# Performance work log

Measured on AMD Instinct MI355X. Metric: run time of the kernel, lower is better.

Reference implementation:

```python
import jax, jax.numpy as jnp
import numpy as np

NUM_EXPERTS = 8
TOP_K = 2
HIDDEN = 1024
INTER = 3584
B, S = 1, 2048


def setup_inputs() -> dict:
    key = jax.random.key(0)
    k0, k1, k2, k3, k4 = jax.random.split(key, 5)
    scale = 0.02
    return {
        "hidden_states": jax.random.normal(k0, (B, S, HIDDEN), dtype=jnp.float32),
        "gate_w": jax.random.normal(k1, (NUM_EXPERTS, HIDDEN), dtype=jnp.float32) * scale,
        "w1": jax.random.normal(k2, (NUM_EXPERTS, INTER, HIDDEN), dtype=jnp.float32) * scale,
        "w2": jax.random.normal(k3, (NUM_EXPERTS, HIDDEN, INTER), dtype=jnp.float32) * scale,
        "w3": jax.random.normal(k4, (NUM_EXPERTS, INTER, HIDDEN), dtype=jnp.float32) * scale,
    }


def reference(hidden_states, gate_w, w1, w2, w3):
    b, s, h = hidden_states.shape
    x = hidden_states.reshape(-1, h)  # [T, H]
    T = x.shape[0]

    # Router: softmax in float32, take top-k, renormalize (normalize_routing_weights=1)
    router_logits = x @ gate_w.T  # [T, E]
    routing_probs = jax.nn.softmax(router_logits.astype(jnp.float32), axis=-1)
    top_w, top_i = jax.lax.top_k(routing_probs, TOP_K)  # [T, K]
    top_w = top_w / jnp.sum(top_w, axis=-1, keepdims=True)
    top_w = top_w.astype(x.dtype)

    # Dense per-token gate matrix [T, E]: weight if expert selected, else 0.
    rows = jnp.arange(T)[:, None]
    gates = jnp.zeros((T, NUM_EXPERTS), dtype=x.dtype).at[rows, top_i].set(top_w)

    # Equivalent to gather-MLP-scatter: y = sum_e gate[:,e] * SwiGLU_e(x)
    out = jnp.zeros((T, h), dtype=x.dtype)
    for e in range(NUM_EXPERTS):
        hid = jax.nn.silu(x @ w1[e].T) * (x @ w3[e].T)  # [T, F]
        out = out + (hid @ w2[e].T) * gates[:, e:e + 1]
    return out.reshape(b, s, h)
```

## Files before the change

### kernel.cpp

```cpp
#include <hip/hip_runtime.h>
#include <hip/hip_bf16.h>
#include <stdint.h>

#define T_TOKENS 2048
#define HID_DIM 1024
#define INTER 3584
#define NEXP 8
#define PTILES 40

typedef float f32x4 __attribute__((ext_vector_type(4)));
typedef short short8 __attribute__((ext_vector_type(8)));
typedef unsigned short ushort8 __attribute__((ext_vector_type(8)));

#define AS1 __attribute__((address_space(1)))
#define AS3 __attribute__((address_space(3)))

__device__ __forceinline__ void gload_lds16(const void* g, void* l) {
    __builtin_amdgcn_global_load_lds((AS1 void*)g, (AS3 void*)l, 16, 0, 0);
}

__device__ __forceinline__ f32x4 mfma16(short8 a, short8 b, f32x4 c) {
    return __builtin_amdgcn_mfma_f32_16x16x32_bf16(a, b, c, 0, 0, 0);
}

__device__ __forceinline__ unsigned short f2bf(float f) {
    union { __hip_bfloat16 h; unsigned short u; } cv;
    cv.h = __float2bfloat16(f);
    return cv.u;
}

__device__ __forceinline__ ushort8 cvt8(float4 v0, float4 v1) {
    ushort8 u;
    u[0] = f2bf(v0.x); u[1] = f2bf(v0.y); u[2] = f2bf(v0.z); u[3] = f2bf(v0.w);
    u[4] = f2bf(v1.x); u[5] = f2bf(v1.y); u[6] = f2bf(v1.z); u[7] = f2bf(v1.w);
    return u;
}

__global__ __launch_bounds__(256) void cvt_k(const float* __restrict__ w1, const float* __restrict__ w2,
                                             const float* __restrict__ w3,
                                             unsigned short* __restrict__ w1b,
                                             unsigned short* __restrict__ w2b,
                                             unsigned short* __restrict__ w3b) {
    const float* src;
    unsigned short* dst;
    if (blockIdx.z == 0) { src = w1; dst = w1b; }
    else if (blockIdx.z == 1) { src = w3; dst = w3b; }
    else { src = w2; dst = w2b; }
    size_t i = ((size_t)blockIdx.x * 256 + threadIdx.x) * 16;
    float4 v0 = *reinterpret_cast<const float4*>(src + i);
    float4 v1 = *reinterpret_cast<const float4*>(src + i + 4);
    float4 v2 = *reinterpret_cast<const float4*>(src + i + 8);
    float4 v3 = *reinterpret_cast<const float4*>(src + i + 12);
    *reinterpret_cast<ushort8*>(dst + i) = cvt8(v0, v1);
    *reinterpret_cast<ushort8*>(dst + i + 8) = cvt8(v2, v3);
}

__global__ void router_k(const float* __restrict__ x, const float* __restrict__ gw,
                         int* __restrict__ topk_e, float* __restrict__ topk_w,
                         int* __restrict__ ctl) {
    int lane = threadIdx.x & 63;
    int wid = threadIdx.x >> 6;
    int t = blockIdx.x * 4 + wid;
    const float* xr = x + (size_t)t * HID_DIM;

    float acc[NEXP];
#pragma unroll
    for (int e = 0; e < NEXP; ++e) acc[e] = 0.f;

#pragma unroll
    for (int j = 0; j < 4; ++j) {
        int c = j * 256 + lane * 4;
        float4 v = *reinterpret_cast<const float4*>(xr + c);
#pragma unroll
        for (int e = 0; e < NEXP; ++e) {
            float4 g = *reinterpret_cast<const float4*>(gw + e * HID_DIM + c);
            acc[e] += v.x * g.x + v.y * g.y + v.z * g.z + v.w * g.w;
        }
    }
#pragma unroll
    for (int off = 32; off > 0; off >>= 1)
#pragma unroll
        for (int e = 0; e < NEXP; ++e) acc[e] += __shfl_xor(acc[e], off, 64);

    if (lane == 0) {
        int e0 = 0;
#pragma unroll
        for (int e = 1; e < NEXP; ++e) if (acc[e] > acc[e0]) e0 = e;
        int e1 = -1;
        float b1 = 0.f;
#pragma unroll
        for (int e = 0; e < NEXP; ++e) {
            if (e == e0) continue;
            if (e1 < 0 || acc[e] > b1) { e1 = e; b1 = acc[e]; }
        }
        float p1 = __expf(b1 - acc[e0]);
        float s = 1.f + p1;
        topk_e[2 * t] = e0; topk_e[2 * t + 1] = e1;
        topk_w[2 * t] = 1.f / s; topk_w[2 * t + 1] = p1 / s;
        atomicAdd(&ctl[e0], 1);
        atomicAdd(&ctl[e1], 1);
    }
}

__global__ void prefix_k(int* __restrict__ ctl) {
    if (threadIdx.x == 0) {
        int r = 0, ns = 0;
        for (int e = 0; e < NEXP; ++e) {
            ctl[32 + e] = r;
            int c = ctl[e];
            r += (c + 127) & ~127;
            ctl[16 + e] = 0;
            int ntm = (c + 127) >> 7;
            for (int tm = 0; tm < ntm; ++tm) ctl[64 + ns++] = (e << 16) | tm;
        }
        ctl[48] = ns;
    }
}

__global__ void scatter_k(const int* __restrict__ topk_e, const float* __restrict__ topk_w,
                          int* __restrict__ ctl, int* __restrict__ perm_token,
                          float* __restrict__ perm_gate) {
    int t = blockIdx.x * 256 + threadIdx.x;
    if (t >= T_TOKENS) return;
#pragma unroll
    for (int k = 0; k < 2; ++k) {
        int e = topk_e[2 * t + k];
        int p = ctl[32 + e] + atomicAdd(&ctl[16 + e], 1);
        perm_token[p] = t;
        perm_gate[p] = topk_w[2 * t + k];
    }
}

__global__ __launch_bounds__(256) void pack_x_k(const float* __restrict__ x,
                                                const int* __restrict__ perm_token,
                                                unsigned short* __restrict__ xgp) {
    int ptile = blockIdx.x;
    int kt = blockIdx.y;
    int row = threadIdx.x & 127;
    int kh = threadIdx.x >> 7;
    int tok = perm_token[ptile * 128 + row];
    const float* s = x + (size_t)tok * HID_DIM + kt * 64 + kh * 32;
    unsigned short* d = xgp + (size_t)ptile * 131072 + (size_t)kt * 8192;
#pragma unroll
    for (int kb2 = 0; kb2 < 4; ++kb2) {
        int kb = kh * 4 + kb2;
        float4 v0 = *reinterpret_cast<const float4*>(s + kb2 * 8);
        float4 v1 = *reinterpret_cast<const float4*>(s + kb2 * 8 + 4);
        *reinterpret_cast<ushort8*>(d + (kb * 128 + row) * 8) = cvt8(v0, v1);
    }
}

__global__ __launch_bounds__(512, 4) void gemm1_k(
    const unsigned short* __restrict__ xgp,
    const unsigned short* __restrict__ w1b, const unsigned short* __restrict__ w3b,
    const int* __restrict__ ctl, unsigned short* __restrict__ hidp) {
    int ns = ctl[48];
    int nt = blockIdx.x >> 3;
    int slot = (blockIdx.x & 7) * 5 + blockIdx.y;
    if (slot >= ns) return;
    int et = ctl[64 + slot];
    int e = et >> 16, tm = et & 0xffff;
    int cnt = ctl[e];
    int off = ctl[32 + e];
    int ptile = (off >> 7) + tm;

    __shared__ __attribute__((aligned(16))) unsigned short A_l[8192];
    __shared__ __attribute__((aligned(16))) unsigned short B1_l[8192];
    __shared__ __attribute__((aligned(16))) unsigned short B3_l[8192];

    int tid = threadIdx.x;
    int lane = tid & 63;
    int wid = tid >> 6;
    int wr = wid >> 2, wc = wid & 3;
    int q = lane >> 4, rr = lane & 15;

    const unsigned short* asrc = xgp + (size_t)ptile * 131072;

    int col0 = tid >> 3;
    int c0 = tid & 7;
    int swzc = c0 ^ (col0 & 7);
    size_t rowbase = (size_t)(e * INTER + nt * 128) * HID_DIM;
    const unsigned short* b1r = w1b + rowbase + (size_t)col0 * HID_DIM + swzc * 8;
    const unsigned short* b3r = w3b + rowbase + (size_t)col0 * HID_DIM + swzc * 8;

    f32x4 acc1[4][2], acc3[4][2];
#pragma unroll
    for (int i = 0; i < 4; ++i)
#pragma unroll
        for (int j = 0; j < 2; ++j) { acc1[i][j] = 0.f; acc3[i][j] = 0.f; }

    for (int kt = 0; kt < 16; ++kt) {
        const unsigned short* as_ = asrc + (size_t)kt * 8192;
        gload_lds16(as_ + tid * 8, A_l + tid * 8);
        gload_lds16(as_ + (512 + tid) * 8, A_l + (512 + tid) * 8);
        gload_lds16(b1r + kt * 64, B1_l + tid * 8);
        gload_lds16(b1r + (size_t)64 * HID_DIM + kt * 64, B1_l + (512 + tid) * 8);
        gload_lds16(b3r + kt * 64, B3_l + tid * 8);
        gload_lds16(b3r + (size_t)64 * HID_DIM + kt * 64, B3_l + (512 + tid) * 8);
        __syncthreads();
#pragma unroll
        for (int kk = 0; kk < 2; ++kk) {
            short8 a[4], b1v[2], b3v[2];
            const unsigned short* abase = A_l + ((kk * 4 + q) * 128 + wr * 64 + rr) * 8;
#pragma unroll
            for (int i = 0; i < 4; ++i) a[i] = *reinterpret_cast<const short8*>(abase + i * 128);
            int swz = ((kk * 4 + q) ^ (rr & 7)) * 8;
            const unsigned short* b1base = B1_l + (wc * 32 + rr) * 64 + swz;
            const unsigned short* b3base = B3_l + (wc * 32 + rr) * 64 + swz;
#pragma unroll
            for (int j = 0; j < 2; ++j) {
                b1v[j] = *reinterpret_cast<const short8*>(b1base + j * 1024);
                b3v[j] = *reinterpret_cast<const short8*>(b3base + j * 1024);
            }
#pragma unroll
            for (int i = 0; i < 4; ++i)
#pragma unroll
                for (int j = 0; j < 2; ++j) {
                    acc1[i][j] = mfma16(a[i], b1v[j], acc1[i][j]);
                    acc3[i][j] = mfma16(a[i], b3v[j], acc3[i][j]);
                }
        }
        __syncthreads();
    }

    int rbase = wr * 64 + q * 4;
#pragma unroll
    for (int i = 0; i < 4; ++i) {
#pragma unroll
        for (int r = 0; r < 4; ++r) {
            int lrow = rbase + i * 16 + r;
            if (tm * 128 + lrow < cnt) {
#pragma unroll
                for (int j = 0; j < 2; ++j) {
                    int cw = wc * 32 + j * 16 + rr;
                    int tile = nt * 2 + (cw >> 6);
                    int cl = cw & 63;
                    float g = acc1[i][j][r];
                    float u = acc3[i][j][r];
                    float h = (g / (1.f + __expf(-g))) * u;
                    hidp[(size_t)(ptile * 56 + tile) * 8192 + ((cl >> 3) * 128 + lrow) * 8 + (cl & 7)] = f2bf(h);
                }
            }
        }
    }
}

__global__ __launch_bounds__(256) void gemm2_k(
    const unsigned short* __restrict__ hidp, const unsigned short* __restrict__ w2b,
    const int* __restrict__ ctl, const int* __restrict__ perm_token,
    const float* __restrict__ perm_gate, float* __restrict__ out) {
    int ns = ctl[48];
    int nty = blockIdx.x >> 3;
    int slot = (blockIdx.x & 7) * 5 + blockIdx.y;
    if (slot >= ns) return;
    int et = ctl[64 + slot];
    int e = et >> 16, tm = et & 0xffff;
    int ks = blockIdx.z;
    int cnt = ctl[e];
    int off = ctl[32 + e];
    int ptile = (off >> 7) + tm;

    __shared__ __attribute__((aligned(16))) unsigned short A_l[8192];
    __shared__ __attribute__((aligned(16))) unsigned short B_l[8192];

    int tid = threadIdx.x;
    int lane = tid & 63;
    int wid = tid >> 6;
    int wr = wid >> 1, wc = wid & 1;
    int q = lane >> 4, rr = lane & 15;

    const unsigned short* asrc = hidp + (size_t)(ptile * 56) * 8192;

    int colg0 = tid >> 3;
    int c0 = tid & 7;
    int swzc = c0 ^ (colg0 & 7);
    const unsigned short* b2r = w2b + (size_t)(e * HID_DIM + nty * 128 + colg0) * INTER + swzc * 8;

    f32x4 acc[4][4];
#pragma unroll
    for (int i = 0; i < 4; ++i)
#pragma unroll
        for (int j = 0; j < 4; ++j) acc[i][j] = 0.f;

    int kt0 = ks * 28;
    for (int t = 0; t < 28; ++t) {
        int kt = kt0 + t;
        const unsigned short* as_ = asrc + (size_t)kt * 8192;
#pragma unroll
        for (int c = 0; c < 4; ++c)
            gload_lds16(as_ + (c * 256 + tid) * 8, A_l + (c * 256 + tid) * 8);
#pragma unroll
        for (int i = 0; i < 4; ++i)
            gload_lds16(b2r + (size_t)i * 32 * INTER + kt * 64, B_l + (i * 256 + tid) * 8);
        __syncthreads();
#pragma unroll
        for (int kk = 0; kk < 2; ++kk) {
            short8 a[4], b[4];
            const unsigned short* abase = A_l + ((kk * 4 + q) * 128 + wr * 64 + rr) * 8;
            int swz = ((kk * 4 + q) ^ (rr & 7)) * 8;
            const unsigned short* bbase = B_l + wc * 4096 + rr * 64 + swz;
#pragma unroll
            for (int i = 0; i < 4; ++i) a[i] = *reinterpret_cast<const short8*>(abase + i * 128);
#pragma unroll
            for (int j = 0; j < 4; ++j) b[j] = *reinterpret_cast<const short8*>(bbase + j * 1024);
#pragma unroll
            for (int i = 0; i < 4; ++i)
#pragma unroll
                for (int j = 0; j < 4; ++j) acc[i][j] = mfma16(a[i], b[j], acc[i][j]);
        }
        __syncthreads();
    }

    int rb = wr * 64 + q * 4;
    int hb = nty * 128 + wc * 64 + rr;
#pragma unroll
    for (int i = 0; i < 4; ++i) {
#pragma unroll
        for (int r = 0; r < 4; ++r) {
            int lrow = rb + i * 16 + r;
            int grow = tm * 128 + lrow;
            if (grow < cnt) {
                int p = off + grow;
                int tok = perm_token[p];
                float gate = perm_gate[p];
#pragma unroll
                for (int j = 0; j < 4; ++j)
                    atomicAdd(&out[(size_t)tok * HID_DIM + hb + j * 16], acc[i][j][r] * gate);
            }
        }
    }
}

extern "C" void kernel_launch(void* const* d_in, const int* in_sizes, int n_in,
                              void* d_out, int out_size, void* d_ws, size_t ws_size,
                              hipStream_t stream) {
    const float* x  = (const float*)d_in[0];
    const float* gw = (const float*)d_in[1];
    const float* w1 = (const float*)d_in[2];
    const float* w2 = (const float*)d_in[3];
    const float* w3 = (const float*)d_in[4];
    float* out = (float*)d_out;

    char* ws = (char*)d_ws;
    int*   ctl        = (int*)ws;
    int*   topk_e     = (int*)(ws + 4096);
    float* topk_w     = (float*)(ws + 20480);
    int*   perm_token = (int*)(ws + 36864);
    float* perm_gate  = (float*)(ws + 57344);
    unsigned short* xgp  = (unsigned short*)(ws + (1ull << 20));
    unsigned short* hidp = (unsigned short*)(ws + 12582912);
    unsigned short* w1b  = (unsigned short*)(ws + 52428800);
    unsigned short* w3b  = (unsigned short*)(ws + 111149056);
    unsigned short* w2b  = (unsigned short*)(ws + 169869312);

    hipMemsetAsync(ctl, 0, 512, stream);
    hipMemsetAsync(perm_token, 0, PTILES * 128 * sizeof(int), stream);
    hipMemsetAsync(out, 0, (size_t)out_size * sizeof(float), stream);

    cvt_k<<<dim3(7168, 1, 3), 256, 0, stream>>>(w1, w2, w3, w1b, w2b, w3b);
    router_k<<<dim3(T_TOKENS / 4), 256, 0, stream>>>(x, gw, topk_e, topk_w, ctl);
    prefix_k<<<dim3(1), 64, 0, stream>>>(ctl);
    scatter_k<<<dim3(T_TOKENS / 256), 256, 0, stream>>>(topk_e, topk_w, ctl, perm_token, perm_gate);
    pack_x_k<<<dim3(PTILES, 16), 256, 0, stream>>>(x, perm_token, xgp);
    gemm1_k<<<dim3(224, 5), 512, 0, stream>>>(xgp, w1b, w3b, ctl, hidp);
    gemm2_k<<<dim3(64, 5, 2), 256, 0, stream>>>(hidp, w2b, ctl, perm_token, perm_gate, out);
}
```

Before: 341.0 us.

## Double-buffer LDS in both expert GEMMs with half-depth K steps and more split-K

Both expert GEMM kernels now use two LDS buffers, each holding a 32-wide K slice. Each step issues the global-to-LDS load for the next slice before computing on the current one, and a manual vmcnt wait plus raw s_barrier replaces the full __syncthreads pair. The B tile layout drops the XOR swizzle for a plain 32-element row stride, and launch bounds are raised for occupancy. gemm2 goes from 2 to 4 K-splits. This trades more float atomics on the output and possible LDS bank conflicts from the unswizzled layout for load/compute overlap and more resident blocks.

```diff
diff --git a/kernel.cpp b/kernel.cpp
--- a/kernel.cpp
+++ b/kernel.cpp
@@ -150,7 +150,7 @@
     }
 }
 
-__global__ __launch_bounds__(512, 4) void gemm1_k(
+__global__ __launch_bounds__(512, 6) void gemm1_k(
     const unsigned short* __restrict__ xgp,
     const unsigned short* __restrict__ w1b, const unsigned short* __restrict__ w3b,
     const int* __restrict__ ctl, unsigned short* __restrict__ hidp) {
@@ -164,9 +164,9 @@
     int off = ctl[32 + e];
     int ptile = (off >> 7) + tm;
 
-    __shared__ __attribute__((aligned(16))) unsigned short A_l[8192];
-    __shared__ __attribute__((aligned(16))) unsigned short B1_l[8192];
-    __shared__ __attribute__((aligned(16))) unsigned short B3_l[8192];
+    __shared__ __attribute__((aligned(16))) unsigned short A_l[2 * 4096];
+    __shared__ __attribute__((aligned(16))) unsigned short B1_l[2 * 4096];
+    __shared__ __attribute__((aligned(16))) unsigned short B3_l[2 * 4096];
 
     int tid = threadIdx.x;
     int lane = tid & 63;
@@ -176,12 +176,11 @@
 
     const unsigned short* asrc = xgp + (size_t)ptile * 131072;
 
-    int col0 = tid >> 3;
-    int c0 = tid & 7;
-    int swzc = c0 ^ (col0 & 7);
+    int colb = tid >> 2;
+    int c4 = tid & 3;
     size_t rowbase = (size_t)(e * INTER + nt * 128) * HID_DIM;
-    const unsigned short* b1r = w1b + rowbase + (size_t)col0 * HID_DIM + swzc * 8;
-    const unsigned short* b3r = w3b + rowbase + (size_t)col0 * HID_DIM + swzc * 8;
+    const unsigned short* b1r = w1b + rowbase + (size_t)colb * HID_DIM + c4 * 8;
+    const unsigned short* b3r = w3b + rowbase + (size_t)colb * HID_DIM + c4 * 8;
 
     f32x4 acc1[4][2], acc3[4][2];
 #pragma unroll
@@ -189,28 +188,36 @@
 #pragma unroll
         for (int j = 0; j < 2; ++j) { acc1[i][j] = 0.f; acc3[i][j] = 0.f; }
 
-    for (int kt = 0; kt < 16; ++kt) {
-        const unsigned short* as_ = asrc + (size_t)kt * 8192;
-        gload_lds16(as_ + tid * 8, A_l + tid * 8);
-        gload_lds16(as_ + (512 + tid) * 8, A_l + (512 + tid) * 8);
-        gload_lds16(b1r + kt * 64, B1_l + tid * 8);
-        gload_lds16(b1r + (size_t)64 * HID_DIM + kt * 64, B1_l + (512 + tid) * 8);
-        gload_lds16(b3r + kt * 64, B3_l + tid * 8);
-        gload_lds16(b3r + (size_t)64 * HID_DIM + kt * 64, B3_l + (512 + tid) * 8);
-        __syncthreads();
-#pragma unroll
-        for (int kk = 0; kk < 2; ++kk) {
+#define G1_STAGE(BUF, T) do {                                                    \
+        int t_ = (T);                                                            \
+        const unsigned short* as_ = asrc + (t_ >> 1) * 8192 + (t_ & 1) * 4096;   \
+        gload_lds16(as_ + tid * 8, A_l + (BUF) * 4096 + tid * 8);                \
+        gload_lds16(b1r + t_ * 32, B1_l + (BUF) * 4096 + tid * 8);               \
+        gload_lds16(b3r + t_ * 32, B3_l + (BUF) * 4096 + tid * 8);               \
+    } while (0)
+
+    G1_STAGE(0, 0);
+    int buf = 0;
+    for (int t = 0; t < 32; ++t) {
+        if (t < 31) {
+            G1_STAGE(buf ^ 1, t + 1);
+            asm volatile("s_waitcnt vmcnt(3)" ::: "memory");
+        } else {
+            asm volatile("s_waitcnt vmcnt(0)" ::: "memory");
+        }
+        __builtin_amdgcn_sched_barrier(0);
+        __builtin_amdgcn_s_barrier();
+        {
             short8 a[4], b1v[2], b3v[2];
-            const unsigned short* abase = A_l + ((kk * 4 + q) * 128 + wr * 64 + rr) * 8;
+            const unsigned short* abase = A_l + buf * 4096 + (q * 128 + wr * 64 + rr) * 8;
 #pragma unroll
             for (int i = 0; i < 4; ++i) a[i] = *reinterpret_cast<const short8*>(abase + i * 128);
-            int swz = ((kk * 4 + q) ^ (rr & 7)) * 8;
-            const unsigned short* b1base = B1_l + (wc * 32 + rr) * 64 + swz;
-            const unsigned short* b3base = B3_l + (wc * 32 + rr) * 64 + swz;
+            const unsigned short* b1base = B1_l + buf * 4096 + (wc * 32 + rr) * 32 + q * 8;
+            const unsigned short* b3base = B3_l + buf * 4096 + (wc * 32 + rr) * 32 + q * 8;
 #pragma unroll
             for (int j = 0; j < 2; ++j) {
-                b1v[j] = *reinterpret_cast<const short8*>(b1base + j * 1024);
-                b3v[j] = *reinterpret_cast<const short8*>(b3base + j * 1024);
+                b1v[j] = *reinterpret_cast<const short8*>(b1base + j * 512);
+                b3v[j] = *reinterpret_cast<const short8*>(b3base + j * 512);
             }
 #pragma unroll
             for (int i = 0; i < 4; ++i)
@@ -220,8 +227,10 @@
                     acc3[i][j] = mfma16(a[i], b3v[j], acc3[i][j]);
                 }
         }
-        __syncthreads();
-    }
+        __builtin_amdgcn_s_barrier();
+        buf ^= 1;
+    }
+#undef G1_STAGE
 
     int rbase = wr * 64 + q * 4;
 #pragma unroll
@@ -245,7 +254,7 @@
     }
 }
 
-__global__ __launch_bounds__(256) void gemm2_k(
+__global__ __launch_bounds__(256, 4) void gemm2_k(
     const unsigned short* __restrict__ hidp, const unsigned short* __restrict__ w2b,
     const int* __restrict__ ctl, const int* __restrict__ perm_token,
     const float* __restrict__ perm_gate, float* __restrict__ out) {
@@ -260,8 +269,8 @@
     int off = ctl[32 + e];
     int ptile = (off >> 7) + tm;
 
-    __shared__ __attribute__((aligned(16))) unsigned short A_l[8192];
-    __shared__ __attribute__((aligned(16))) unsigned short B_l[8192];
+    __shared__ __attribute__((aligned(16))) unsigned short A_l[2 * 4096];
+    __shared__ __attribute__((aligned(16))) unsigned short B_l[2 * 4096];
 
     int tid = threadIdx.x;
     int lane = tid & 63;
@@ -270,11 +279,7 @@
     int q = lane >> 4, rr = lane & 15;
 
     const unsigned short* asrc = hidp + (size_t)(ptile * 56) * 8192;
-
-    int colg0 = tid >> 3;
-    int c0 = tid & 7;
-    int swzc = c0 ^ (colg0 & 7);
-    const unsigned short* b2r = w2b + (size_t)(e * HID_DIM + nty * 128 + colg0) * INTER + swzc * 8;
+    const unsigned short* b2base_g = w2b + (size_t)(e * HID_DIM + nty * 128) * INTER;
 
     f32x4 acc[4][4];
 #pragma unroll
@@ -282,34 +287,47 @@
 #pragma unroll
         for (int j = 0; j < 4; ++j) acc[i][j] = 0.f;
 
-    int kt0 = ks * 28;
+#define G2_STAGE(BUF, G) do {                                                        \
+        int g_ = (G);                                                                \
+        const unsigned short* as_ = asrc + (size_t)(g_ >> 1) * 8192 + (g_ & 1) * 4096; \
+        gload_lds16(as_ + tid * 8, A_l + (BUF) * 4096 + tid * 8);                    \
+        gload_lds16(as_ + (256 + tid) * 8, A_l + (BUF) * 4096 + (256 + tid) * 8);    \
+        int d0_ = tid, d1_ = 256 + tid;                                              \
+        gload_lds16(b2base_g + (size_t)(d0_ >> 2) * INTER + g_ * 32 + (d0_ & 3) * 8, \
+                    B_l + (BUF) * 4096 + d0_ * 8);                                   \
+        gload_lds16(b2base_g + (size_t)(d1_ >> 2) * INTER + g_ * 32 + (d1_ & 3) * 8, \
+                    B_l + (BUF) * 4096 + d1_ * 8);                                   \
+    } while (0)
+
+    int g0 = ks * 28;
+    G2_STAGE(0, g0);
+    int buf = 0;
     for (int t = 0; t < 28; ++t) {
-        int kt = kt0 + t;
-        const unsigned short* as_ = asrc + (size_t)kt * 8192;
-#pragma unroll
-        for (int c = 0; c < 4; ++c)
-            gload_lds16(as_ + (c * 256 + tid) * 8, A_l + (c * 256 + tid) * 8);
-#pragma unroll
-        for (int i = 0; i < 4; ++i)
-            gload_lds16(b2r + (size_t)i * 32 * INTER + kt * 64, B_l + (i * 256 + tid) * 8);
-        __syncthreads();
-#pragma unroll
-        for (int kk = 0; kk < 2; ++kk) {
+        if (t < 27) {
+            G2_STAGE(buf ^ 1, g0 + t + 1);
+            asm volatile("s_waitcnt vmcnt(4)" ::: "memory");
+        } else {
+            asm volatile("s_waitcnt vmcnt(0)" ::: "memory");
+        }
+        __builtin_amdgcn_sched_barrier(0);
+        __builtin_amdgcn_s_barrier();
+        {
             short8 a[4], b[4];
-            const unsigned short* abase = A_l + ((kk * 4 + q) * 128 + wr * 64 + rr) * 8;
-            int swz = ((kk * 4 + q) ^ (rr & 7)) * 8;
-            const unsigned short* bbase = B_l + wc * 4096 + rr * 64 + swz;
+            const unsigned short* abase = A_l + buf * 4096 + (q * 128 + wr * 64 + rr) * 8;
+            const unsigned short* bbase = B_l + buf * 4096 + (wc * 64 + rr) * 32 + q * 8;
 #pragma unroll
             for (int i = 0; i < 4; ++i) a[i] = *reinterpret_cast<const short8*>(abase + i * 128);
 #pragma unroll
-            for (int j = 0; j < 4; ++j) b[j] = *reinterpret_cast<const short8*>(bbase + j * 1024);
+            for (int j = 0; j < 4; ++j) b[j] = *reinterpret_cast<const short8*>(bbase + j * 512);
 #pragma unroll
             for (int i = 0; i < 4; ++i)
 #pragma unroll
                 for (int j = 0; j < 4; ++j) acc[i][j] = mfma16(a[i], b[j], acc[i][j]);
         }
-        __syncthreads();
-    }
+        __builtin_amdgcn_s_barrier();
+        buf ^= 1;
+    }
+#undef G2_STAGE
 
     int rb = wr * 64 + q * 4;
     int hb = nty * 128 + wc * 64 + rr;
@@ -363,5 +381,5 @@
     scatter_k<<<dim3(T_TOKENS / 256), 256, 0, stream>>>(topk_e, topk_w, ctl, perm_token, perm_gate);
     pack_x_k<<<dim3(PTILES, 16), 256, 0, stream>>>(x, perm_token, xgp);
     gemm1_k<<<dim3(224, 5), 512, 0, stream>>>(xgp, w1b, w3b, ctl, hidp);
-    gemm2_k<<<dim3(64, 5, 2), 256, 0, stream>>>(hidp, w2b, ctl, perm_token, perm_gate, out);
-}
+    gemm2_k<<<dim3(64, 5, 4), 256, 0, stream>>>(hidp, w2b, ctl, perm_token, perm_gate, out);
+}
```

New measurement: 764.2 us. +124.1%, slower.

## Double-buffer gemm1 LDS tiles with K=32 stages and async prefetch

Applied to the files above, without the earlier changes.

Splits the gemm1 K loop into 32 half-size stages and double-buffers the A, B1 and B3 LDS tiles. The next stage is prefetched with global_load_lds while the current one is consumed, gated by s_waitcnt vmcnt and raw barriers. The goal is to overlap global-memory latency with MFMA work instead of stalling at every sync. In exchange it drops the XOR swizzle on B tiles, which may add LDS bank conflicts, and doubles the number of barriers.

```diff
diff --git a/kernel.cpp b/kernel.cpp
--- a/kernel.cpp
+++ b/kernel.cpp
@@ -164,9 +164,9 @@
     int off = ctl[32 + e];
     int ptile = (off >> 7) + tm;
 
-    __shared__ __attribute__((aligned(16))) unsigned short A_l[8192];
-    __shared__ __attribute__((aligned(16))) unsigned short B1_l[8192];
-    __shared__ __attribute__((aligned(16))) unsigned short B3_l[8192];
+    __shared__ __attribute__((aligned(16))) unsigned short A_l[2 * 4096];
+    __shared__ __attribute__((aligned(16))) unsigned short B1_l[2 * 4096];
+    __shared__ __attribute__((aligned(16))) unsigned short B3_l[2 * 4096];
 
     int tid = threadIdx.x;
     int lane = tid & 63;
@@ -176,12 +176,11 @@
 
     const unsigned short* asrc = xgp + (size_t)ptile * 131072;
 
-    int col0 = tid >> 3;
-    int c0 = tid & 7;
-    int swzc = c0 ^ (col0 & 7);
+    int colb = tid >> 2;
+    int c4 = tid & 3;
     size_t rowbase = (size_t)(e * INTER + nt * 128) * HID_DIM;
-    const unsigned short* b1r = w1b + rowbase + (size_t)col0 * HID_DIM + swzc * 8;
-    const unsigned short* b3r = w3b + rowbase + (size_t)col0 * HID_DIM + swzc * 8;
+    const unsigned short* b1r = w1b + rowbase + (size_t)colb * HID_DIM + c4 * 8;
+    const unsigned short* b3r = w3b + rowbase + (size_t)colb * HID_DIM + c4 * 8;
 
     f32x4 acc1[4][2], acc3[4][2];
 #pragma unroll
@@ -189,28 +188,36 @@
 #pragma unroll
         for (int j = 0; j < 2; ++j) { acc1[i][j] = 0.f; acc3[i][j] = 0.f; }
 
-    for (int kt = 0; kt < 16; ++kt) {
-        const unsigned short* as_ = asrc + (size_t)kt * 8192;
-        gload_lds16(as_ + tid * 8, A_l + tid * 8);
-        gload_lds16(as_ + (512 + tid) * 8, A_l + (512 + tid) * 8);
-        gload_lds16(b1r + kt * 64, B1_l + tid * 8);
-        gload_lds16(b1r + (size_t)64 * HID_DIM + kt * 64, B1_l + (512 + tid) * 8);
-        gload_lds16(b3r + kt * 64, B3_l + tid * 8);
-        gload_lds16(b3r + (size_t)64 * HID_DIM + kt * 64, B3_l + (512 + tid) * 8);
-        __syncthreads();
-#pragma unroll
-        for (int kk = 0; kk < 2; ++kk) {
+#define G1_STAGE(BUF, T) do {                                                    \
+        int t_ = (T);                                                            \
+        const unsigned short* as_ = asrc + (t_ >> 1) * 8192 + (t_ & 1) * 4096;   \
+        gload_lds16(as_ + tid * 8, A_l + (BUF) * 4096 + tid * 8);                \
+        gload_lds16(b1r + t_ * 32, B1_l + (BUF) * 4096 + tid * 8);               \
+        gload_lds16(b3r + t_ * 32, B3_l + (BUF) * 4096 + tid * 8);               \
+    } while (0)
+
+    G1_STAGE(0, 0);
+    int buf = 0;
+    for (int t = 0; t < 32; ++t) {
+        if (t < 31) {
+            G1_STAGE(buf ^ 1, t + 1);
+            asm volatile("s_waitcnt vmcnt(3)" ::: "memory");
+        } else {
+            asm volatile("s_waitcnt vmcnt(0)" ::: "memory");
+        }
+        __builtin_amdgcn_sched_barrier(0);
+        __builtin_amdgcn_s_barrier();
+        {
             short8 a[4], b1v[2], b3v[2];
-            const unsigned short* abase = A_l + ((kk * 4 + q) * 128 + wr * 64 + rr) * 8;
+            const unsigned short* abase = A_l + buf * 4096 + (q * 128 + wr * 64 + rr) * 8;
 #pragma unroll
             for (int i = 0; i < 4; ++i) a[i] = *reinterpret_cast<const short8*>(abase + i * 128);
-            int swz = ((kk * 4 + q) ^ (rr & 7)) * 8;
-            const unsigned short* b1base = B1_l + (wc * 32 + rr) * 64 + swz;
-            const unsigned short* b3base = B3_l + (wc * 32 + rr) * 64 + swz;
+            const unsigned short* b1base = B1_l + buf * 4096 + (wc * 32 + rr) * 32 + q * 8;
+            const unsigned short* b3base = B3_l + buf * 4096 + (wc * 32 + rr) * 32 + q * 8;
 #pragma unroll
             for (int j = 0; j < 2; ++j) {
-                b1v[j] = *reinterpret_cast<const short8*>(b1base + j * 1024);
-                b3v[j] = *reinterpret_cast<const short8*>(b3base + j * 1024);
+                b1v[j] = *reinterpret_cast<const short8*>(b1base + j * 512);
+                b3v[j] = *reinterpret_cast<const short8*>(b3base + j * 512);
             }
 #pragma unroll
             for (int i = 0; i < 4; ++i)
@@ -220,8 +227,10 @@
                     acc3[i][j] = mfma16(a[i], b3v[j], acc3[i][j]);
                 }
         }
-        __syncthreads();
-    }
+        __builtin_amdgcn_s_barrier();
+        buf ^= 1;
+    }
+#undef G1_STAGE
 
     int rbase = wr * 64 + q * 4;
 #pragma unroll
```

Measured after the change: 345.8 us. No clear change (+1.4%).
